# Kernel optimization log

Hardware: AMD Instinct MI355X
Metric: run time of the kernel (lower is better)

The kernel has to match this reference:

```python
import jax, jax.numpy as jnp
import numpy as np

N_POINTS = 1440   # number of detector angles (thetas)
N_INT = 4000      # trapezoid integration samples along each ray
N_GRID = 4096     # SoS field is (N_GRID, N_GRID)
GRID_LO, GRID_HI = -0.06, 0.06
R_BODY = 0.05
V0 = 1500.0


def setup_inputs() -> dict:
    key = jax.random.key(0)
    k1, k2, k3 = jax.random.split(key, 3)
    # query point strictly inside the body circle (r < R_body)
    x = jnp.float32(0.012)
    y = jnp.float32(-0.007)
    # speed-of-sound field ~ water SoS with heterogeneity, strictly positive
    SoS = (1480.0 + 40.0 * jax.random.uniform(k3, (N_GRID, N_GRID))).astype(jnp.float32)
    thetas = jnp.linspace(0.0, 2.0 * jnp.pi, N_POINTS, dtype=jnp.float32).reshape(-1, 1)
    steps = jnp.linspace(0.0, 1.0, N_INT, dtype=jnp.float32).reshape(1, -1)
    x_vec = jnp.linspace(GRID_LO, GRID_HI, N_GRID, dtype=jnp.float32)
    dx = x_vec[1] - x_vec[0]
    return {
        "x": x, "y": y, "SoS": SoS,
        "thetas": thetas, "steps": steps,
        "x0": x_vec[0], "y0": x_vec[0], "dx": dx, "dy": dx,
        "R_body": jnp.float32(R_BODY), "v0": jnp.float32(V0),
    }


def reference(x, y, SoS, thetas, steps, x0, y0, dx, dy, R_body, v0):
    # polar coords of query point; note torch code uses atan2(x, y)
    r = jnp.sqrt(x * x + y * y)
    phi = jnp.arctan2(x, y)
    s = r * jnp.sin(thetas - phi)                      # (P,1)
    arg = jnp.maximum(R_body * R_body - s * s, 0.0)    # shared, >0 when r<R_body
    sqrt_arg = jnp.sqrt(arg)
    l_in = sqrt_arg + r * jnp.cos(thetas - phi)
    l_out = 2.0 * sqrt_arg * (jnp.cos(phi - thetas) >= 0.0).astype(sqrt_arg.dtype)
    l = jnp.where(r < R_body, l_in, l_out)             # (P,1) chord lengths

    xs = l * steps                                     # (P,N) arc-length samples
    px = x - xs * jnp.sin(thetas)                      # (P,N) sample positions
    py = y - xs * jnp.cos(thetas)
    x_index = jnp.round((px - x0) / dx).astype(jnp.int32)
    y_index = jnp.round((py - y0) / dy).astype(jnp.int32)
    # gather: negative row index (-y_index) wraps from the end, as in torch/numpy
    vals = 1.0 - v0 / SoS[-y_index, x_index]           # (P,N)
    # trapezoid over non-uniformly labeled x = l*steps (uniform per row)
    dseg = jnp.diff(xs, axis=1)                        # (P,N-1)
    wf = jnp.sum(0.5 * (vals[:, :-1] + vals[:, 1:]) * dseg, axis=1)
    return thetas.reshape(-1), wf
```

## Files before the change

### kernel.cpp

```cpp
#include <hip/hip_runtime.h>

#define N_POINTS 1440
#define N_INT    4000
#define N_GRID   4096
#define BLOCK    256

#define NSEG     4
#define SEG_LEN  (N_INT / NSEG)
#define RPC      4
#define NCLUST   (N_POINTS / RPC)
#define K_FULL   15
#define TAIL_Q   (SEG_LEN - K_FULL * 64)

__global__ __launch_bounds__(BLOCK, 6) void wavefront_partial_kernel(
    const float* __restrict__ xp,
    const float* __restrict__ yp,
    const float* __restrict__ SoS,
    const float* __restrict__ thetas,
    const float* __restrict__ x0p,
    const float* __restrict__ y0p,
    const float* __restrict__ dxp,
    const float* __restrict__ dyp,
    const float* __restrict__ Rp,
    const float* __restrict__ v0p,
    float* __restrict__ ws)
{
    const int b = blockIdx.x;
    const int c = b >> 2;
    const int S = ((b & 3) + c) & 3;
    const int t = threadIdx.x;
    const int r = t & 3;
    const int q = t >> 2;

    const int p = c * RPC + r;

    const float x  = xp[0];
    const float y  = yp[0];
    const float x0 = x0p[0];
    const float y0 = y0p[0];
    const float dx = dxp[0];
    const float dy = dyp[0];
    const float Rb = Rp[0];
    const float v0 = v0p[0];

    const float theta = thetas[p];

    const float rr  = sqrtf(x * x + y * y);
    const float phi = atan2f(x, y);
    const float st  = sinf(theta);
    const float ct  = cosf(theta);

    const float sv    = rr * sinf(theta - phi);
    const float arg   = fmaxf(Rb * Rb - sv * sv, 0.0f);
    const float sq    = sqrtf(arg);
    const float l_in  = sq + rr * cosf(theta - phi);
    const float l_out = 2.0f * sq * (cosf(phi - theta) >= 0.0f ? 1.0f : 0.0f);
    const float l     = (rr < Rb) ? l_in : l_out;

    const float ds = 1.0f / 3999.0f;
    const float Ax = (x - x0) / dx;
    const float Ay = (y - y0) / dy;
    const float bx = l * st / dx * ds;
    const float by = l * ct / dy * ds;

    const int   jb  = S * SEG_LEN + q;
    const float fx0 = fmaf(-bx, (float)jb, Ax + 0.5f);
    const float gy0 = fmaf( by, (float)jb, 4096.5f - Ay);
    const float dX  = -bx * 64.0f;
    const float dY  =  by * 64.0f;

    const bool has_tail = (q < TAIL_Q);

    float rv[16];
#pragma unroll
    for (int k = 0; k < K_FULL; ++k) {
        const float kf = (float)k;
        const int xi  = (int)fmaf(kf, dX, fx0);
        const int row = (int)fmaf(kf, dY, gy0);
        rv[k] = SoS[(row << 12) + xi];
    }
    if (has_tail) {
        const float kf = (float)K_FULL;
        const int xi  = (int)fmaf(kf, dX, fx0);
        const int row = (int)fmaf(kf, dY, gy0);
        rv[15] = SoS[(row << 12) + xi];
    }

    float accR = 0.0f;
#pragma unroll
    for (int k = 0; k < K_FULL; ++k)
        accR += __builtin_amdgcn_rcpf(rv[k]);
    float n = 15.0f;
    if (has_tail) { accR += __builtin_amdgcn_rcpf(rv[15]); n = 16.0f; }

    if (S == 0 && q == 0) {
        accR -= 0.5f * __builtin_amdgcn_rcpf(rv[0]);
        n -= 0.5f;
    }
    if (S == NSEG - 1 && q == TAIL_Q - 1) {
        accR -= 0.5f * __builtin_amdgcn_rcpf(rv[15]);
        n -= 0.5f;
    }

    float acc = fmaf(-v0, accR, n);

    acc += __shfl_xor(acc, 4, 64);
    acc += __shfl_xor(acc, 8, 64);
    acc += __shfl_xor(acc, 16, 64);
    acc += __shfl_xor(acc, 32, 64);

    __shared__ float wsum[4][4];
    if ((t & 63) < 4) wsum[t >> 6][r] = acc;
    __syncthreads();
    if (t < 4) {
        const float tot = (wsum[0][t] + wsum[1][t]) + (wsum[2][t] + wsum[3][t]);
        ws[(c * RPC + t) * NSEG + S] = tot;
    }
}

__global__ __launch_bounds__(BLOCK) void wavefront_combine_kernel(
    const float* __restrict__ xp,
    const float* __restrict__ yp,
    const float* __restrict__ thetas,
    const float* __restrict__ Rp,
    const float* __restrict__ ws,
    float* __restrict__ out)
{
    const int p = blockIdx.x * BLOCK + threadIdx.x;
    if (p >= N_POINTS) return;

    const float x  = xp[0];
    const float y  = yp[0];
    const float Rb = Rp[0];
    const float theta = thetas[p];

    const float rr  = sqrtf(x * x + y * y);
    const float phi = atan2f(x, y);
    const float sv    = rr * sinf(theta - phi);
    const float arg   = fmaxf(Rb * Rb - sv * sv, 0.0f);
    const float sq    = sqrtf(arg);
    const float l_in  = sq + rr * cosf(theta - phi);
    const float l_out = 2.0f * sq * (cosf(phi - theta) >= 0.0f ? 1.0f : 0.0f);
    const float l     = (rr < Rb) ? l_in : l_out;

    const float4 a = *(const float4*)(ws + p * NSEG);
    const float tot = (a.x + a.y) + (a.z + a.w);

    out[p] = theta;
    out[N_POINTS + p] = l * (1.0f / 3999.0f) * tot;
}

extern "C" void kernel_launch(void* const* d_in, const int* in_sizes, int n_in,
                              void* d_out, int out_size, void* d_ws, size_t ws_size,
                              hipStream_t stream) {
    (void)in_sizes; (void)n_in; (void)out_size; (void)ws_size;

    const float* xp     = (const float*)d_in[0];
    const float* yp     = (const float*)d_in[1];
    const float* SoS    = (const float*)d_in[2];
    const float* thetas = (const float*)d_in[3];
    const float* x0p    = (const float*)d_in[5];
    const float* y0p    = (const float*)d_in[6];
    const float* dxp    = (const float*)d_in[7];
    const float* dyp    = (const float*)d_in[8];
    const float* Rp     = (const float*)d_in[9];
    const float* v0p    = (const float*)d_in[10];

    float* ws  = (float*)d_ws;
    float* out = (float*)d_out;

    wavefront_partial_kernel<<<NCLUST * NSEG, BLOCK, 0, stream>>>(
        xp, yp, SoS, thetas, x0p, y0p, dxp, dyp, Rp, v0p, ws);
    wavefront_combine_kernel<<<(N_POINTS + BLOCK - 1) / BLOCK, BLOCK, 0, stream>>>(
        xp, yp, thetas, Rp, ws, out);
}
```

Before: 117.6 us.

## Fuse partial and combine kernels into one block-per-ray kernel

Replaces the two-kernel scheme, where each block handled 4 rays split into 4 segments plus a separate combine pass, with one kernel where each block integrates one full ray. It reduces via a full wavefront shuffle and writes the final output directly. This removes the second launch and the workspace round trip. It also changes the gather pattern so lanes in a wavefront sample consecutive points of the same ray, but it gives up the segment staggering across blocks.

Result: slower. 125.0 us (+6.3%).

```diff
diff --git a/kernel.cpp b/kernel.cpp
--- a/kernel.cpp
+++ b/kernel.cpp
@@ -5,14 +5,10 @@
 #define N_GRID   4096
 #define BLOCK    256
 
-#define NSEG     4
-#define SEG_LEN  (N_INT / NSEG)
-#define RPC      4
-#define NCLUST   (N_POINTS / RPC)
 #define K_FULL   15
-#define TAIL_Q   (SEG_LEN - K_FULL * 64)
+#define TAIL_T   (N_INT - K_FULL * BLOCK)
 
-__global__ __launch_bounds__(BLOCK, 6) void wavefront_partial_kernel(
+__global__ __launch_bounds__(BLOCK, 6) void wavefront_sos_kernel(
     const float* __restrict__ xp,
     const float* __restrict__ yp,
     const float* __restrict__ SoS,
@@ -23,16 +19,10 @@
     const float* __restrict__ dyp,
     const float* __restrict__ Rp,
     const float* __restrict__ v0p,
-    float* __restrict__ ws)
+    float* __restrict__ out)
 {
-    const int b = blockIdx.x;
-    const int c = b >> 2;
-    const int S = ((b & 3) + c) & 3;
+    const int p = blockIdx.x;
     const int t = threadIdx.x;
-    const int r = t & 3;
-    const int q = t >> 2;
-
-    const int p = c * RPC + r;
 
     const float x  = xp[0];
     const float y  = yp[0];
@@ -63,13 +53,12 @@
     const float bx = l * st / dx * ds;
     const float by = l * ct / dy * ds;
 
-    const int   jb  = S * SEG_LEN + q;
-    const float fx0 = fmaf(-bx, (float)jb, Ax + 0.5f);
-    const float gy0 = fmaf( by, (float)jb, 4096.5f - Ay);
-    const float dX  = -bx * 64.0f;
-    const float dY  =  by * 64.0f;
+    const float fx0 = fmaf(-bx, (float)t, Ax + 0.5f);
+    const float gy0 = fmaf( by, (float)t, 4096.5f - Ay);
+    const float dX  = -bx * 256.0f;
+    const float dY  =  by * 256.0f;
 
-    const bool has_tail = (q < TAIL_Q);
+    const bool has_tail = (t < TAIL_T);
 
     float rv[16];
 #pragma unroll
@@ -93,67 +82,40 @@
     float n = 15.0f;
     if (has_tail) { accR += __builtin_amdgcn_rcpf(rv[15]); n = 16.0f; }
 
-    if (S == 0 && q == 0) {
+    if (t == 0) {
         accR -= 0.5f * __builtin_amdgcn_rcpf(rv[0]);
         n -= 0.5f;
     }
-    if (S == NSEG - 1 && q == TAIL_Q - 1) {
+    if (t == TAIL_T - 1) {
         accR -= 0.5f * __builtin_amdgcn_rcpf(rv[15]);
         n -= 0.5f;
     }
 
     float acc = fmaf(-v0, accR, n);
 
+    acc += __shfl_xor(acc, 1, 64);
+    acc += __shfl_xor(acc, 2, 64);
     acc += __shfl_xor(acc, 4, 64);
     acc += __shfl_xor(acc, 8, 64);
     acc += __shfl_xor(acc, 16, 64);
     acc += __shfl_xor(acc, 32, 64);
 
-    __shared__ float wsum[4][4];
-    if ((t & 63) < 4) wsum[t >> 6][r] = acc;
+    __shared__ float wave_sums[4];
+    if ((t & 63) == 0) wave_sums[t >> 6] = acc;
     __syncthreads();
-    if (t < 4) {
-        const float tot = (wsum[0][t] + wsum[1][t]) + (wsum[2][t] + wsum[3][t]);
-        ws[(c * RPC + t) * NSEG + S] = tot;
+
+    if (t == 0) {
+        const float total = (wave_sums[0] + wave_sums[1])
+                          + (wave_sums[2] + wave_sums[3]);
+        out[p] = theta;
+        out[N_POINTS + p] = l * ds * total;
     }
-}
-
-__global__ __launch_bounds__(BLOCK) void wavefront_combine_kernel(
-    const float* __restrict__ xp,
-    const float* __restrict__ yp,
-    const float* __restrict__ thetas,
-    const float* __restrict__ Rp,
-    const float* __restrict__ ws,
-    float* __restrict__ out)
-{
-    const int p = blockIdx.x * BLOCK + threadIdx.x;
-    if (p >= N_POINTS) return;
-
-    const float x  = xp[0];
-    const float y  = yp[0];
-    const float Rb = Rp[0];
-    const float theta = thetas[p];
-
-    const float rr  = sqrtf(x * x + y * y);
-    const float phi = atan2f(x, y);
-    const float sv    = rr * sinf(theta - phi);
-    const float arg   = fmaxf(Rb * Rb - sv * sv, 0.0f);
-    const float sq    = sqrtf(arg);
-    const float l_in  = sq + rr * cosf(theta - phi);
-    const float l_out = 2.0f * sq * (cosf(phi - theta) >= 0.0f ? 1.0f : 0.0f);
-    const float l     = (rr < Rb) ? l_in : l_out;
-
-    const float4 a = *(const float4*)(ws + p * NSEG);
-    const float tot = (a.x + a.y) + (a.z + a.w);
-
-    out[p] = theta;
-    out[N_POINTS + p] = l * (1.0f / 3999.0f) * tot;
 }
 
 extern "C" void kernel_launch(void* const* d_in, const int* in_sizes, int n_in,
                               void* d_out, int out_size, void* d_ws, size_t ws_size,
                               hipStream_t stream) {
-    (void)in_sizes; (void)n_in; (void)out_size; (void)ws_size;
+    (void)in_sizes; (void)n_in; (void)out_size; (void)d_ws; (void)ws_size;
 
     const float* xp     = (const float*)d_in[0];
     const float* yp     = (const float*)d_in[1];
@@ -166,11 +128,8 @@
     const float* Rp     = (const float*)d_in[9];
     const float* v0p    = (const float*)d_in[10];
 
-    float* ws  = (float*)d_ws;
     float* out = (float*)d_out;
 
-    wavefront_partial_kernel<<<NCLUST * NSEG, BLOCK, 0, stream>>>(
-        xp, yp, SoS, thetas, x0p, y0p, dxp, dyp, Rp, v0p, ws);
-    wavefront_combine_kernel<<<(N_POINTS + BLOCK - 1) / BLOCK, BLOCK, 0, stream>>>(
-        xp, yp, thetas, Rp, ws, out);
+    wavefront_sos_kernel<<<N_POINTS, BLOCK, 0, stream>>>(
+        xp, yp, SoS, thetas, x0p, y0p, dxp, dyp, Rp, v0p, out);
 }
```

## Fuse partial and combine kernels using last-block atomic counter reduction

Applied to the files above, without the earlier changes.

Merges the two-kernel pipeline into a single launch. Each block publishes its already-scaled partial sum with a release store and increments a global counter, and the last block to arrive reads all partials and writes the final output. This removes the second kernel launch and its per-point trig recomputation. In exchange every block pays an atomic and an extra barrier, and the final combine runs serially in one block.

New measurement: 197.1 us. 67.6% more time.

```diff
diff --git a/kernel.cpp b/kernel.cpp
--- a/kernel.cpp
+++ b/kernel.cpp
@@ -9,10 +9,13 @@
 #define SEG_LEN  (N_INT / NSEG)
 #define RPC      4
 #define NCLUST   (N_POINTS / RPC)
+#define NBLOCKS  (NCLUST * NSEG)
 #define K_FULL   15
 #define TAIL_Q   (SEG_LEN - K_FULL * 64)
 
-__global__ __launch_bounds__(BLOCK, 6) void wavefront_partial_kernel(
+__device__ int g_done = 0;
+
+__global__ __launch_bounds__(BLOCK, 6) void wavefront_fused_kernel(
     const float* __restrict__ xp,
     const float* __restrict__ yp,
     const float* __restrict__ SoS,
@@ -23,7 +26,8 @@
     const float* __restrict__ dyp,
     const float* __restrict__ Rp,
     const float* __restrict__ v0p,
-    float* __restrict__ ws)
+    float* __restrict__ ws,
+    float* __restrict__ out)
 {
     const int b = blockIdx.x;
     const int c = b >> 2;
@@ -113,41 +117,38 @@
     if ((t & 63) < 4) wsum[t >> 6][r] = acc;
     __syncthreads();
     if (t < 4) {
-        const float tot = (wsum[0][t] + wsum[1][t]) + (wsum[2][t] + wsum[3][t]);
-        ws[(c * RPC + t) * NSEG + S] = tot;
+        const float tot = ((wsum[0][t] + wsum[1][t]) + (wsum[2][t] + wsum[3][t]))
+                        * (l * ds);
+        __hip_atomic_store(&ws[(c * RPC + t) * NSEG + S], tot,
+                           __ATOMIC_RELEASE, __HIP_MEMORY_SCOPE_AGENT);
     }
-}
+    __syncthreads();
 
-__global__ __launch_bounds__(BLOCK) void wavefront_combine_kernel(
-    const float* __restrict__ xp,
-    const float* __restrict__ yp,
-    const float* __restrict__ thetas,
-    const float* __restrict__ Rp,
-    const float* __restrict__ ws,
-    float* __restrict__ out)
-{
-    const int p = blockIdx.x * BLOCK + threadIdx.x;
-    if (p >= N_POINTS) return;
+    __shared__ int is_last;
+    if (t == 0) {
+        const int old = __hip_atomic_fetch_add(&g_done, 1,
+                            __ATOMIC_ACQ_REL, __HIP_MEMORY_SCOPE_AGENT);
+        is_last = (old == NBLOCKS - 1);
+        if (is_last)
+            __hip_atomic_store(&g_done, 0,
+                               __ATOMIC_RELAXED, __HIP_MEMORY_SCOPE_AGENT);
+    }
+    __syncthreads();
 
-    const float x  = xp[0];
-    const float y  = yp[0];
-    const float Rb = Rp[0];
-    const float theta = thetas[p];
-
-    const float rr  = sqrtf(x * x + y * y);
-    const float phi = atan2f(x, y);
-    const float sv    = rr * sinf(theta - phi);
-    const float arg   = fmaxf(Rb * Rb - sv * sv, 0.0f);
-    const float sq    = sqrtf(arg);
-    const float l_in  = sq + rr * cosf(theta - phi);
-    const float l_out = 2.0f * sq * (cosf(phi - theta) >= 0.0f ? 1.0f : 0.0f);
-    const float l     = (rr < Rb) ? l_in : l_out;
-
-    const float4 a = *(const float4*)(ws + p * NSEG);
-    const float tot = (a.x + a.y) + (a.z + a.w);
-
-    out[p] = theta;
-    out[N_POINTS + p] = l * (1.0f / 3999.0f) * tot;
+    if (is_last) {
+        for (int i = t; i < N_POINTS; i += BLOCK) {
+            const float s0 = __hip_atomic_load(&ws[i * NSEG + 0],
+                                 __ATOMIC_RELAXED, __HIP_MEMORY_SCOPE_AGENT);
+            const float s1 = __hip_atomic_load(&ws[i * NSEG + 1],
+                                 __ATOMIC_RELAXED, __HIP_MEMORY_SCOPE_AGENT);
+            const float s2 = __hip_atomic_load(&ws[i * NSEG + 2],
+                                 __ATOMIC_RELAXED, __HIP_MEMORY_SCOPE_AGENT);
+            const float s3 = __hip_atomic_load(&ws[i * NSEG + 3],
+                                 __ATOMIC_RELAXED, __HIP_MEMORY_SCOPE_AGENT);
+            out[i] = thetas[i];
+            out[N_POINTS + i] = (s0 + s1) + (s2 + s3);
+        }
+    }
 }
 
 extern "C" void kernel_launch(void* const* d_in, const int* in_sizes, int n_in,
@@ -169,8 +170,6 @@
     float* ws  = (float*)d_ws;
     float* out = (float*)d_out;
 
-    wavefront_partial_kernel<<<NCLUST * NSEG, BLOCK, 0, stream>>>(
-        xp, yp, SoS, thetas, x0p, y0p, dxp, dyp, Rp, v0p, ws);
-    wavefront_combine_kernel<<<(N_POINTS + BLOCK - 1) / BLOCK, BLOCK, 0, stream>>>(
-        xp, yp, thetas, Rp, ws, out);
+    wavefront_fused_kernel<<<NBLOCKS, BLOCK, 0, stream>>>(
+        xp, yp, SoS, thetas, x0p, y0p, dxp, dyp, Rp, v0p, ws, out);
 }
```
